# Performance work log

Measured on AMD Instinct MI355X. Metric: run time of the kernel, lower is better.

## Reference

```python
import jax, jax.numpy as jnp
import numpy as np

N_NODES = 50000
N_REL = 256
D_IN = 128
NHID = 128
NHEADS = 2
D_OUT = NHID * NHEADS  # 256
ALPHA = 0.2  # leakyrelu slope


def _l2norm(x, eps=1e-12):
    n = jnp.sqrt(jnp.sum(x * x, axis=1, keepdims=True))
    return x / jnp.maximum(n, eps)


def _gat_layer(x, edge, edge_embed, a, a2, num_nodes, concat):
    """KBGAT-style sparse attention layer.
    x: [N, d_in]; edge: [2, E] (row0=dst, row1=src); edge_embed: [E, d_rel]
    a: [d_out, 2*d_in + d_rel]; a2: [d_out].
    Returns (h, h_raw, rowsum) ~ (x, x_l, x_w) of the original layer.
    """
    d_in = x.shape[1]
    dst, src = edge[0], edge[1]
    # edge_m = a @ cat(x[dst], x[src], edge_embed).T, computed blockwise -> [E, d_out]
    a_d, a_s, a_r = a[:, :d_in], a[:, d_in:2 * d_in], a[:, 2 * d_in:]
    edge_m = x[dst] @ a_d.T + x[src] @ a_s.T + edge_embed @ a_r.T
    # attention logits: exp(-leakyrelu(a2 . edge_m))
    powers = -jax.nn.leaky_relu(edge_m @ a2, negative_slope=ALPHA)  # [E]
    edge_e = jnp.exp(powers)
    rowsum = jax.ops.segment_sum(edge_e, dst, num_segments=num_nodes)  # [N]
    rowsum = jnp.where(rowsum == 0, 1e-12, rowsum)
    h_raw = jax.ops.segment_sum(edge_e[:, None] * edge_m, dst, num_segments=num_nodes)  # [N, d_out]
    h = h_raw / rowsum[:, None]
    if concat:
        h = jax.nn.elu(h)
    return h, h_raw, rowsum[:, None]


def setup_inputs() -> dict:
    key = jax.random.key(0)
    ks = jax.random.split(key, 16)
    E, E_NHOP = 300000, 30000
    xav = lambda k, shp: jax.random.uniform(k, shp, jnp.float32, -1.0, 1.0) * (
        1.414 * np.sqrt(6.0 / (shp[-2] + shp[-1])))
    inp = {
        "entity_embeddings": jax.random.normal(ks[0], (N_NODES, D_IN), jnp.float32),
        "relation_embeddings": jax.random.normal(ks[1], (N_REL, D_IN), jnp.float32),
        # per-head layer-1 attention params (stacked over heads)
        "a1": xav(ks[2], (NHEADS, NHID, 2 * D_IN + D_IN)),
        "a2_1": xav(ks[3], (NHEADS, NHID)),
        "W": xav(ks[4], (D_IN, D_OUT)),          # relation projection in SpGAT
        "a_out": xav(ks[5], (D_OUT, 2 * D_OUT + D_OUT)),
        "a2_out": xav(ks[6], (1, D_OUT))[0],
        "W_entities": xav(ks[7], (D_IN, D_OUT)),
        "batch_inputs": jax.random.randint(ks[8], (4096, 3), 0, N_NODES),
        "edge_list": jax.random.randint(ks[9], (2, E), 0, N_NODES),
        "edge_type": jax.random.randint(ks[10], (E,), 0, N_REL),
        "edge_list_nhop": jax.random.randint(ks[11], (2, E_NHOP), 0, N_NODES),
        "edge_type_nhop": jax.random.randint(ks[12], (E_NHOP, 2), 0, N_REL),
    }
    return inp


def reference(entity_embeddings, relation_embeddings, a1, a2_1, W, a_out, a2_out,
              W_entities, batch_inputs, edge_list, edge_type, edge_list_nhop,
              edge_type_nhop):
    # in-place row normalization of entity embeddings (as in original forward)
    ent = _l2norm(entity_embeddings)
    edge_all = jnp.concatenate([edge_list, edge_list_nhop], axis=1)  # [2, E+Enh]

    # ---- SpGAT layer 1: multi-head over original relation embeddings ----
    edge_embed = relation_embeddings[edge_type]
    edge_embed_nhop = relation_embeddings[edge_type_nhop[:, 0]] + relation_embeddings[edge_type_nhop[:, 1]]
    ee_all = jnp.concatenate([edge_embed, edge_embed_nhop], axis=0)
    heads = [
        _gat_layer(ent, edge_all, ee_all, a1[h], a2_1[h], N_NODES, concat=True)[0]
        for h in range(NHEADS)
    ]
    x = jnp.concatenate(heads, axis=1)  # [N, NHEADS*NHID]

    # ---- relation projection + output attention layer ----
    out_relation_1 = relation_embeddings @ W  # [R, D_OUT]
    ee2 = out_relation_1[edge_type]
    ee2_nhop = out_relation_1[edge_type_nhop[:, 0]] + out_relation_1[edge_type_nhop[:, 1]]
    ee2_all = jnp.concatenate([ee2, ee2_nhop], axis=0)
    xo, x_l, x_w = _gat_layer(x, edge_all, ee2_all, a_out, a2_out, N_NODES, concat=False)
    xo, x_l, x_w = jax.nn.elu(xo), jax.nn.elu(x_l), jax.nn.elu(x_w)

    # ---- residual mask update + normalization ----
    mask = jnp.zeros((N_NODES,), xo.dtype).at[batch_inputs[:, 2]].set(1.0)
    entities_upgraded = ent @ W_entities
    out_entity_1 = entities_upgraded + mask[:, None] * xo
    out_entity_1 = _l2norm(out_entity_1)
    out_entity_l_1 = _l2norm(x_l)
    return (out_entity_1, out_relation_1, out_entity_l_1)
```

## Files before the change

### kernel.cpp

```cpp
#include <hip/hip_runtime.h>
#include <hip/hip_bf16.h>
#include <math.h>

#define N_NODES 50000
#define E1 300000
#define EN 30000
#define ETOT 330000

typedef __hip_bfloat16 bf16;

__device__ __forceinline__ float b2f(bf16 x){ return __bfloat162float(x); }
__device__ __forceinline__ bf16 f2b(float x){ return __float2bfloat16(x); }

__device__ __forceinline__ float ldf(const void* p, long i, bool f32){
  return f32 ? ((const float*)p)[i] : b2f(((const bf16*)p)[i]);
}
__device__ __forceinline__ void stf(void* p, long i, float v, bool f32){
  if (f32) ((float*)p)[i] = v; else ((bf16*)p)[i] = f2b(v);
}
__device__ __forceinline__ void stv4(void* p, long elem, float a, float b,
                                     float c, float d, bool f32){
  if (f32){
    float4 t; t.x=a; t.y=b; t.z=c; t.w=d;
    *reinterpret_cast<float4*>((float*)p + elem) = t;
  } else {
    bf16 t[4] = {f2b(a), f2b(b), f2b(c), f2b(d)};
    *reinterpret_cast<uint2*>((bf16*)p + elem) = *reinterpret_cast<uint2*>(t);
  }
}

template<int NT>
__device__ __forceinline__ float block_sum(float v){
  __shared__ float sm[NT/64];
  #pragma unroll
  for (int o=32;o>0;o>>=1) v += __shfl_down(v,o);
  if ((threadIdx.x & 63)==0) sm[threadIdx.x>>6] = v;
  __syncthreads();
  float t = 0.f;
  #pragma unroll
  for (int w=0;w<NT/64;w++) t += sm[w];
  __syncthreads();
  return t;
}

__global__ void k_detect(const void* __restrict__ emb, int* __restrict__ flag){
  const unsigned short* h = (const unsigned short*)emb;
  int sane = 0;
  for (int i=0;i<128;i++){
    unsigned e = (h[i]>>7)&0xFFu;
    if (e>=112u && e<=143u) sane++;
  }
  *flag = (sane >= 112) ? 0 : 1;
}

__global__ void k_hist(const int* __restrict__ el, const int* __restrict__ eln,
                       int* __restrict__ cnt){
  int i = blockIdx.x*blockDim.x + threadIdx.x;
  if (i < ETOT){
    int dst = (i < E1) ? el[i] : eln[i - E1];
    atomicAdd(cnt + dst, 1);
  }
}

__global__ __launch_bounds__(1024) void k_scan(const int* __restrict__ cnt,
                                               int* __restrict__ rowp,
                                               int* __restrict__ cur){
  __shared__ int part[1024];
  int t = threadIdx.x;
  const int CH = (N_NODES + 1023)/1024;
  int base = t*CH;
  int s = 0;
  for (int i=0;i<CH;i++){ int n = base+i; if (n < N_NODES) s += cnt[n]; }
  part[t] = s;
  __syncthreads();
  for (int o=1;o<1024;o<<=1){
    int u = (t>=o) ? part[t-o] : 0;
    __syncthreads();
    part[t] += u;
    __syncthreads();
  }
  int off = part[t] - s;
  for (int i=0;i<CH;i++){
    int n = base+i;
    if (n < N_NODES){ rowp[n] = off; cur[n] = off; off += cnt[n]; }
  }
  if (t==0) rowp[N_NODES] = ETOT;
}

__global__ void k_fill(const int* __restrict__ el, const int* __restrict__ et,
                       const int* __restrict__ eln, const int* __restrict__ etn,
                       int* __restrict__ cur, int* __restrict__ esrc,
                       int* __restrict__ epak){
  int i = blockIdx.x*blockDim.x + threadIdx.x;
  if (i >= ETOT) return;
  int dst, src, pk;
  if (i < E1){
    dst = el[i]; src = el[E1 + i];
    pk = et[i];
  } else {
    int e = i - E1;
    dst = eln[e]; src = eln[EN + e];
    pk = etn[2*e] | (etn[2*e+1]<<9) | (1<<18);
  }
  int pos = atomicAdd(cur + dst, 1);
  esrc[pos] = src; epak[pos] = pk;
}

__global__ __launch_bounds__(256) void k_gath1(
    const int* __restrict__ rowp, const int* __restrict__ esrc,
    const int* __restrict__ epak,
    const float* __restrict__ pd, const float* __restrict__ ps,
    const float* __restrict__ rp,
    const float* __restrict__ sd, const float* __restrict__ ss,
    const float* __restrict__ sr,
    float* __restrict__ x, int hoff){
  int w = threadIdx.x >> 6, lane = threadIdx.x & 63;
  int n = blockIdx.x*4 + w;
  if (n >= N_NODES) return;
  const float2* ps2 = (const float2*)ps;
  const float2* rp2 = (const float2*)rp;
  float2 acc; acc.x = 0.f; acc.y = 0.f;
  float rs = 0.f;
  float sdn = sd[n];
  int b = rowp[n], e = rowp[n+1];
  for (int i=b;i<e;i++){
    int src = esrc[i], pk = epak[i];
    int t0 = pk & 511, t1 = (pk>>9)&511, has2 = (pk>>18)&1;
    float srv = sr[t0] + (has2 ? sr[t1] : 0.f);
    float score = sdn + ss[src] + srv;
    float lr = score > 0.f ? score : 0.2f*score;
    float wgt = expf(-lr);
    rs += wgt;
    float2 v  = ps2[(long)src*64 + lane];
    float2 r1 = rp2[(long)t0*64 + lane];
    v.x += r1.x; v.y += r1.y;
    if (has2){ float2 r2v = rp2[(long)t1*64 + lane]; v.x += r2v.x; v.y += r2v.y; }
    acc.x += wgt*v.x; acc.y += wgt*v.y;
  }
  float denom = (rs == 0.f) ? 1e-12f : rs;
  float2 pdv = ((const float2*)pd)[(long)n*64 + lane];
  float hr0 = rs*pdv.x + acc.x, hr1 = rs*pdv.y + acc.y;
  float h0 = hr0/denom; h0 = h0 > 0.f ? h0 : (expf(h0) - 1.f);
  float h1 = hr1/denom; h1 = h1 > 0.f ? h1 : (expf(h1) - 1.f);
  float2 o; o.x = h0; o.y = h1;
  *reinterpret_cast<float2*>(x + (long)n*256 + hoff + lane*2) = o;
}

__global__ __launch_bounds__(256) void k_gath2(
    const int* __restrict__ rowp, const int* __restrict__ esrc,
    const int* __restrict__ epak,
    const float* __restrict__ p2d, const float* __restrict__ ps,
    const float* __restrict__ rp,
    const float* __restrict__ sd, const float* __restrict__ ss,
    const float* __restrict__ sr,
    const float* __restrict__ eu, const float* __restrict__ mask,
    const int* __restrict__ flag, void* __restrict__ out){
  bool f32 = flag[0] != 0;
  int w = threadIdx.x >> 6, lane = threadIdx.x & 63;
  int n = blockIdx.x*4 + w;
  if (n >= N_NODES) return;
  const float4* ps4 = (const float4*)ps;
  const float4* rp4 = (const float4*)rp;
  float4 acc; acc.x=acc.y=acc.z=acc.w=0.f;
  float rs = 0.f;
  float sdn = sd[n];
  int b = rowp[n], e = rowp[n+1];
  for (int i=b;i<e;i++){
    int src = esrc[i], pk = epak[i];
    int t0 = pk & 511, t1 = (pk>>9)&511, has2 = (pk>>18)&1;
    float srv = sr[t0] + (has2 ? sr[t1] : 0.f);
    float score = sdn + ss[src] + srv;
    float lr = score > 0.f ? score : 0.2f*score;
    float wgt = expf(-lr);
    rs += wgt;
    float4 v  = ps4[(long)src*64 + lane];
    float4 r1 = rp4[(long)t0*64 + lane];
    v.x += r1.x; v.y += r1.y; v.z += r1.z; v.w += r1.w;
    if (has2){
      float4 r2v = rp4[(long)t1*64 + lane];
      v.x += r2v.x; v.y += r2v.y; v.z += r2v.z; v.w += r2v.w;
    }
    acc.x += wgt*v.x; acc.y += wgt*v.y; acc.z += wgt*v.z; acc.w += wgt*v.w;
  }
  float denom = (rs == 0.f) ? 1e-12f : rs;
  float mk = mask[n];
  float4 pdv = ((const float4*)p2d)[(long)n*64 + lane];
  float4 euv = ((const float4*)eu)[(long)n*64 + lane];
  float av[4] = {acc.x, acc.y, acc.z, acc.w};
  float pv[4] = {pdv.x, pdv.y, pdv.z, pdv.w};
  float ev[4] = {euv.x, euv.y, euv.z, euv.w};
  float val[4], xl[4];
  float n1 = 0.f, n2 = 0.f;
  #pragma unroll
  for (int m=0;m<4;m++){
    float hr = rs*pv[m] + av[m];
    float xo = hr/denom; xo = xo > 0.f ? xo : (expf(xo) - 1.f);
    float l  = hr > 0.f ? hr : (expf(hr) - 1.f);
    float v  = ev[m] + mk*xo;
    val[m] = v; xl[m] = l;
    n1 += v*v; n2 += l*l;
  }
  #pragma unroll
  for (int o=32;o>0;o>>=1){ n1 += __shfl_xor(n1,o); n2 += __shfl_xor(n2,o); }
  float i1 = 1.f/fmaxf(sqrtf(n1), 1e-12f);
  float i2 = 1.f/fmaxf(sqrtf(n2), 1e-12f);
  stv4(out, (long)n*256 + lane*4,
       val[0]*i1, val[1]*i1, val[2]*i1, val[3]*i1, f32);
  stv4(out, 12865536L + (long)n*256 + lane*4,
       xl[0]*i2, xl[1]*i2, xl[2]*i2, xl[3]*i2, f32);
}

__global__ void k_rel2(const void* __restrict__ rel, const void* __restrict__ W,
                       const int* __restrict__ flag,
                       float* __restrict__ r2, void* __restrict__ out){
  bool f32 = flag[0] != 0;
  int t = blockIdx.x, j = threadIdx.x;
  __shared__ float rs_[128];
  if (j < 128) rs_[j] = ldf(rel, (long)t*128 + j, f32);
  __syncthreads();
  float acc = 0.f;
  #pragma unroll 4
  for (int k=0;k<128;k++) acc += rs_[k]*ldf(W, (long)k*256 + j, f32);
  r2[(long)t*256+j] = acc;
  stf(out, 12800000L + (long)t*256 + j, acc, f32);
}

__global__ void k_trF(const void* __restrict__ src, const int* __restrict__ flag,
                      long bias, long jstride, int J, float* __restrict__ dst){
  bool f32 = flag[0] != 0;
  int k = blockIdx.x, j = threadIdx.x;
  dst[(long)k*J + j] = ldf(src, bias + (long)j*jstride + k, f32);
}

__global__ void k_cvtF(const void* __restrict__ src, const int* __restrict__ flag,
                       int n, float* __restrict__ dst){
  bool f32 = flag[0] != 0;
  int i = blockIdx.x*blockDim.x + threadIdx.x;
  if (i < n) dst[i] = ldf(src, i, f32);
}

template<int NT, int K, int BM, int NORM, int DUAL, int SCORE, int XDUAL>
__global__ __launch_bounds__(NT) void k_gnp(
    const void* __restrict__ X, const int* __restrict__ flag, int N,
    const float* __restrict__ WT1, const float* __restrict__ WT2,
    const void* __restrict__ a2, long a2bias,
    float* __restrict__ O1, float* __restrict__ O2,
    float* __restrict__ s1, float* __restrict__ s2, int ldc){
  __shared__ __align__(16) float xs[BM][K];
  __shared__ float rsc[BM];
  const int NW = NT/64;
  __shared__ float red1[BM][NW];
  __shared__ float red2[BM][NW];
  int t = threadIdx.x;
  int n0 = blockIdx.x * BM;
  bool xf32 = XDUAL ? (flag[0] != 0) : true;

  for (int idx = t; idx < BM*K; idx += NT){
    int m = idx / K, k = idx - m*K;
    int n = n0 + m;
    xs[m][k] = (n < N) ? ldf(X, (long)n*K + k, xf32) : 0.f;
  }
  __syncthreads();

  if (NORM){
    const int NPR = NT / BM;
    int r = t / NPR, l = t - r*NPR;
    float ssq = 0.f;
    #pragma unroll
    for (int k = l; k < K; k += NPR){ float v = xs[r][k]; ssq += v*v; }
    #pragma unroll
    for (int o = NPR>>1; o > 0; o >>= 1) ssq += __shfl_xor(ssq, o);
    if (l == 0) rsc[r] = 1.f / fmaxf(sqrtf(ssq), 1e-12f);
    __syncthreads();
    for (int idx = t; idx < BM*K; idx += NT){
      int m = idx / K, k = idx - m*K;
      xs[m][k] *= rsc[m];
    }
    __syncthreads();
  }

  float a1c[BM], a2c[BM];
  #pragma unroll
  for (int m=0;m<BM;m++){ a1c[m]=0.f; a2c[m]=0.f; }
  const float4* xs4 = reinterpret_cast<const float4*>(&xs[0][0]);
  #pragma unroll 2
  for (int k0=0;k0<K;k0+=4){
    float w1a = WT1[(long)(k0+0)*NT + t];
    float w1b = WT1[(long)(k0+1)*NT + t];
    float w1c = WT1[(long)(k0+2)*NT + t];
    float w1d = WT1[(long)(k0+3)*NT + t];
    float w2a=0.f,w2b=0.f,w2c=0.f,w2d=0.f;
    if (DUAL){
      w2a = WT2[(long)(k0+0)*NT + t];
      w2b = WT2[(long)(k0+1)*NT + t];
      w2c = WT2[(long)(k0+2)*NT + t];
      w2d = WT2[(long)(k0+3)*NT + t];
    }
    #pragma unroll
    for (int m=0;m<BM;m++){
      float4 xv = xs4[(m*K + k0) >> 2];
      a1c[m] += xv.x*w1a + xv.y*w1b + xv.z*w1c + xv.w*w1d;
      if (DUAL) a2c[m] += xv.x*w2a + xv.y*w2b + xv.z*w2c + xv.w*w2d;
    }
  }

  #pragma unroll
  for (int m=0;m<BM;m++){
    int n = n0 + m;
    if (n < N){
      O1[(long)n*ldc + t] = a1c[m];
      if (DUAL) O2[(long)n*ldc + t] = a2c[m];
    }
  }

  if (SCORE){
    bool af32 = flag[0] != 0;
    float a2v = ldf(a2, a2bias + t, af32);
    int w = t >> 6, lane = t & 63;
    #pragma unroll
    for (int m=0;m<BM;m++){
      float v1 = a1c[m]*a2v;
      float v2 = DUAL ? a2c[m]*a2v : 0.f;
      #pragma unroll
      for (int o=32;o>0;o>>=1){ v1 += __shfl_down(v1,o); v2 += __shfl_down(v2,o); }
      if (lane==0){ red1[m][w]=v1; red2[m][w]=v2; }
    }
    __syncthreads();
    if (t < BM && n0 + t < N){
      float v1=0.f, v2=0.f;
      #pragma unroll
      for (int ww=0;ww<NW;ww++){ v1+=red1[t][ww]; v2+=red2[t][ww]; }
      s1[n0+t] = v1;
      if (DUAL) s2[n0+t] = v2;
    }
  }
}

__global__ void k_mask(const int* __restrict__ bi, float* __restrict__ mask){
  int i = blockIdx.x*blockDim.x + threadIdx.x;
  if (i < 4096) mask[bi[i*3 + 2]] = 1.f;
}

extern "C" void kernel_launch(void* const* d_in, const int* in_sizes, int n_in,
                              void* d_out, int out_size, void* d_ws, size_t ws_size,
                              hipStream_t stream) {
  const void* emb = d_in[0];
  const void* rel = d_in[1];
  const void* a1b = d_in[2];
  const void* a21 = d_in[3];
  const void* W   = d_in[4];
  const void* aout= d_in[5];
  const void* a2o = d_in[6];
  const void* We  = d_in[7];
  const int* bi   = (const int*)d_in[8];
  const int* el   = (const int*)d_in[9];
  const int* et   = (const int*)d_in[10];
  const int* eln  = (const int*)d_in[11];
  const int* etn  = (const int*)d_in[12];
  float* ws = (float*)d_ws;

  const size_t PD_=0, PS_=6400000;
  const size_t P2D_=0;
  const size_t CNT_=12800000, ROWP_=12860000, ESRC_=12920000, EPAK_=13260000;
  const size_t TW_=19200000;
  const size_t X_=25600000;
  const size_t P2S_=38400000;
  const size_t SD_=51250000, SS_=51300000, S2D_=51350000,
               S2S_=51400000, MK_=51500000,
               RP1_=51550000, SR1_=51590000, R2_=51600000, RP2_=51670000,
               SR2_=51740000, FLAG_=51750000;
  int* flag = (int*)(ws + FLAG_);
  int* cnt  = (int*)(ws + CNT_);
  int* rowp = (int*)(ws + ROWP_);
  int* esrc = (int*)(ws + ESRC_);
  int* epak = (int*)(ws + EPAK_);

  k_detect<<<1,1,0,stream>>>(emb, flag);

  hipMemsetAsync(ws+MK_,  0, (size_t)50000*sizeof(float), stream);
  hipMemsetAsync(cnt,     0, (size_t)50000*sizeof(int), stream);

  k_hist<<<(ETOT+255)/256,256,0,stream>>>(el, eln, cnt);
  k_scan<<<1,1024,0,stream>>>(cnt, rowp, cnt);
  k_fill<<<(ETOT+255)/256,256,0,stream>>>(el, et, eln, etn, cnt, esrc, epak);

  k_trF<<<128,128,0,stream>>>(a1b, flag, 0L,          384L, 128, ws+TW_);
  k_trF<<<128,128,0,stream>>>(a1b, flag, 128L,        384L, 128, ws+TW_+16384);
  k_trF<<<128,128,0,stream>>>(a1b, flag, 49152L,      384L, 128, ws+TW_+32768);
  k_trF<<<128,128,0,stream>>>(a1b, flag, 49152L+128L, 384L, 128, ws+TW_+49152);
  k_trF<<<128,128,0,stream>>>(a1b, flag, 256L,        384L, 128, ws+TW_+65536);
  k_trF<<<128,128,0,stream>>>(a1b, flag, 49152L+256L, 384L, 128, ws+TW_+81920);

  k_gnp<128,128,16,1,1,1,1><<<(N_NODES+15)/16,128,0,stream>>>(
      emb, flag, N_NODES, ws+TW_, ws+TW_+16384, a21, 0L,
      ws+PD_, ws+PS_, ws+SD_, ws+SS_, 128);
  k_gnp<128,128,16,0,0,1,1><<<16,128,0,stream>>>(
      rel, flag, 256, ws+TW_+65536, nullptr, a21, 0L,
      ws+RP1_, nullptr, ws+SR1_, nullptr, 128);
  k_gath1<<<(N_NODES+3)/4,256,0,stream>>>(rowp, esrc, epak,
      ws+PD_, ws+PS_, ws+RP1_, ws+SD_, ws+SS_, ws+SR1_, ws+X_, 0);

  k_gnp<128,128,16,1,1,1,1><<<(N_NODES+15)/16,128,0,stream>>>(
      emb, flag, N_NODES, ws+TW_+32768, ws+TW_+49152, a21, 128L,
      ws+PD_, ws+PS_, ws+SD_, ws+SS_, 128);
  k_gnp<128,128,16,0,0,1,1><<<16,128,0,stream>>>(
      rel, flag, 256, ws+TW_+81920, nullptr, a21, 128L,
      ws+RP1_, nullptr, ws+SR1_, nullptr, 128);
  k_gath1<<<(N_NODES+3)/4,256,0,stream>>>(rowp, esrc, epak,
      ws+PD_, ws+PS_, ws+RP1_, ws+SD_, ws+SS_, ws+SR1_, ws+X_, 128);

  k_rel2<<<256,256,0,stream>>>(rel, W, flag, ws+R2_, d_out);

  k_trF<<<256,256,0,stream>>>(aout, flag, 0L,   768L, 256, ws+TW_);
  k_trF<<<256,256,0,stream>>>(aout, flag, 256L, 768L, 256, ws+TW_+65536);
  k_trF<<<256,256,0,stream>>>(aout, flag, 512L, 768L, 256, ws+TW_+131072);

  k_gnp<256,256,16,0,0,1,0><<<16,256,0,stream>>>(
      ws+R2_, flag, 256, ws+TW_+131072, nullptr, a2o, 0L,
      ws+RP2_, nullptr, ws+SR2_, nullptr, 256);

  k_gnp<256,256,16,0,1,1,0><<<(N_NODES+15)/16,256,0,stream>>>(
      ws+X_, flag, N_NODES, ws+TW_, ws+TW_+65536, a2o, 0L,
      ws+P2D_, ws+P2S_, ws+S2D_, ws+S2S_, 256);

  k_cvtF<<<128,256,0,stream>>>(We, flag, 32768, ws+RP1_);
  k_mask<<<16,256,0,stream>>>(bi, ws+MK_);
  k_gnp<256,128,16,1,0,0,1><<<(N_NODES+15)/16,256,0,stream>>>(
      emb, flag, N_NODES, ws+RP1_, nullptr, nullptr, 0L,
      ws+X_, nullptr, nullptr, nullptr, 256);

  k_gath2<<<(N_NODES+3)/4,256,0,stream>>>(rowp, esrc, epak,
      ws+P2D_, ws+P2S_, ws+RP2_, ws+S2D_, ws+S2S_, ws+SR2_,
      ws+X_, ws+MK_, flag, d_out);
}
```

Baseline: 1.106 ms.

## Register-tile node projection GEMM: split rows across waves, multiple columns per lane

Restructures the dense projection kernel so each wave owns a subset of the block's rows and each lane computes 2 or 4 adjacent output columns. Weights are loaded as float2/float4 vectors, outputs are stored vectorized, and the attention score reduction becomes a single in-wave shuffle with no shared-memory pass or barrier. The intent is to cut redundant shared-memory reads and weight loads per FMA. Layer-1 launches move from 128 to 256 threads. The weight layout is unchanged (row-major by column), so lane-contiguous column groups map directly onto it.

```diff
diff --git a/kernel.cpp b/kernel.cpp
--- a/kernel.cpp
+++ b/kernel.cpp
@@ -239,19 +239,21 @@
   if (i < n) dst[i] = ldf(src, i, f32);
 }
 
-template<int NT, int K, int BM, int NORM, int DUAL, int SCORE, int XDUAL>
+template<int NT, int K, int BM, int NCOL, int NORM, int DUAL, int SCORE, int XDUAL>
 __global__ __launch_bounds__(NT) void k_gnp(
     const void* __restrict__ X, const int* __restrict__ flag, int N,
     const float* __restrict__ WT1, const float* __restrict__ WT2,
     const void* __restrict__ a2, long a2bias,
     float* __restrict__ O1, float* __restrict__ O2,
-    float* __restrict__ s1, float* __restrict__ s2, int ldc){
+    float* __restrict__ s1, float* __restrict__ s2){
+  const int COLS  = 64*NCOL;
+  const int WAVES = NT/64;
+  const int RW    = BM/WAVES;
   __shared__ __align__(16) float xs[BM][K];
   __shared__ float rsc[BM];
-  const int NW = NT/64;
-  __shared__ float red1[BM][NW];
-  __shared__ float red2[BM][NW];
   int t = threadIdx.x;
+  int wv = t >> 6, ln = t & 63;
+  int r0 = wv * RW;
   int n0 = blockIdx.x * BM;
   bool xf32 = XDUAL ? (flag[0] != 0) : true;
 
@@ -279,59 +281,95 @@
     __syncthreads();
   }
 
-  float a1c[BM], a2c[BM];
-  #pragma unroll
-  for (int m=0;m<BM;m++){ a1c[m]=0.f; a2c[m]=0.f; }
-  const float4* xs4 = reinterpret_cast<const float4*>(&xs[0][0]);
-  #pragma unroll 2
+  float a1c[RW][NCOL], a2c[RW][NCOL];
+  #pragma unroll
+  for (int m=0;m<RW;m++)
+    #pragma unroll
+    for (int c=0;c<NCOL;c++){ a1c[m][c]=0.f; a2c[m][c]=0.f; }
+
   for (int k0=0;k0<K;k0+=4){
-    float w1a = WT1[(long)(k0+0)*NT + t];
-    float w1b = WT1[(long)(k0+1)*NT + t];
-    float w1c = WT1[(long)(k0+2)*NT + t];
-    float w1d = WT1[(long)(k0+3)*NT + t];
-    float w2a=0.f,w2b=0.f,w2c=0.f,w2d=0.f;
-    if (DUAL){
-      w2a = WT2[(long)(k0+0)*NT + t];
-      w2b = WT2[(long)(k0+1)*NT + t];
-      w2c = WT2[(long)(k0+2)*NT + t];
-      w2d = WT2[(long)(k0+3)*NT + t];
-    }
-    #pragma unroll
-    for (int m=0;m<BM;m++){
-      float4 xv = xs4[(m*K + k0) >> 2];
-      a1c[m] += xv.x*w1a + xv.y*w1b + xv.z*w1c + xv.w*w1d;
-      if (DUAL) a2c[m] += xv.x*w2a + xv.y*w2b + xv.z*w2c + xv.w*w2d;
-    }
-  }
-
-  #pragma unroll
-  for (int m=0;m<BM;m++){
-    int n = n0 + m;
+    float w1v[4][NCOL], w2v[4][NCOL];
+    #pragma unroll
+    for (int i=0;i<4;i++){
+      const float* p1 = WT1 + (long)(k0+i)*COLS + ln*NCOL;
+      if constexpr (NCOL==4){
+        float4 v = *reinterpret_cast<const float4*>(p1);
+        w1v[i][0]=v.x; w1v[i][1]=v.y; w1v[i][2]=v.z; w1v[i][3]=v.w;
+      } else {
+        float2 v = *reinterpret_cast<const float2*>(p1);
+        w1v[i][0]=v.x; w1v[i][1]=v.y;
+      }
+      if (DUAL){
+        const float* p2 = WT2 + (long)(k0+i)*COLS + ln*NCOL;
+        if constexpr (NCOL==4){
+          float4 v = *reinterpret_cast<const float4*>(p2);
+          w2v[i][0]=v.x; w2v[i][1]=v.y; w2v[i][2]=v.z; w2v[i][3]=v.w;
+        } else {
+          float2 v = *reinterpret_cast<const float2*>(p2);
+          w2v[i][0]=v.x; w2v[i][1]=v.y;
+        }
+      }
+    }
+    #pragma unroll
+    for (int m=0;m<RW;m++){
+      float4 xv = *reinterpret_cast<const float4*>(&xs[r0+m][k0]);
+      #pragma unroll
+      for (int c=0;c<NCOL;c++){
+        a1c[m][c] += xv.x*w1v[0][c] + xv.y*w1v[1][c] + xv.z*w1v[2][c] + xv.w*w1v[3][c];
+        if (DUAL)
+          a2c[m][c] += xv.x*w2v[0][c] + xv.y*w2v[1][c] + xv.z*w2v[2][c] + xv.w*w2v[3][c];
+      }
+    }
+  }
+
+  #pragma unroll
+  for (int m=0;m<RW;m++){
+    int n = n0 + r0 + m;
     if (n < N){
-      O1[(long)n*ldc + t] = a1c[m];
-      if (DUAL) O2[(long)n*ldc + t] = a2c[m];
+      float* o1 = O1 + (long)n*COLS + ln*NCOL;
+      if constexpr (NCOL==4){
+        float4 v; v.x=a1c[m][0]; v.y=a1c[m][1]; v.z=a1c[m][2]; v.w=a1c[m][3];
+        *reinterpret_cast<float4*>(o1) = v;
+      } else {
+        float2 v; v.x=a1c[m][0]; v.y=a1c[m][1];
+        *reinterpret_cast<float2*>(o1) = v;
+      }
+      if (DUAL){
+        float* o2 = O2 + (long)n*COLS + ln*NCOL;
+        if constexpr (NCOL==4){
+          float4 v; v.x=a2c[m][0]; v.y=a2c[m][1]; v.z=a2c[m][2]; v.w=a2c[m][3];
+          *reinterpret_cast<float4*>(o2) = v;
+        } else {
+          float2 v; v.x=a2c[m][0]; v.y=a2c[m][1];
+          *reinterpret_cast<float2*>(o2) = v;
+        }
+      }
     }
   }
 
   if (SCORE){
     bool af32 = flag[0] != 0;
-    float a2v = ldf(a2, a2bias + t, af32);
-    int w = t >> 6, lane = t & 63;
-    #pragma unroll
-    for (int m=0;m<BM;m++){
-      float v1 = a1c[m]*a2v;
-      float v2 = DUAL ? a2c[m]*a2v : 0.f;
+    float a2v[NCOL];
+    #pragma unroll
+    for (int c=0;c<NCOL;c++) a2v[c] = ldf(a2, a2bias + ln*NCOL + c, af32);
+    #pragma unroll
+    for (int m=0;m<RW;m++){
+      float v1 = 0.f, v2 = 0.f;
       #pragma unroll
-      for (int o=32;o>0;o>>=1){ v1 += __shfl_down(v1,o); v2 += __shfl_down(v2,o); }
-      if (lane==0){ red1[m][w]=v1; red2[m][w]=v2; }
-    }
-    __syncthreads();
-    if (t < BM && n0 + t < N){
-      float v1=0.f, v2=0.f;
+      for (int c=0;c<NCOL;c++){
+        v1 += a1c[m][c]*a2v[c];
+        if (DUAL) v2 += a2c[m][c]*a2v[c];
+      }
       #pragma unroll
-      for (int ww=0;ww<NW;ww++){ v1+=red1[t][ww]; v2+=red2[t][ww]; }
-      s1[n0+t] = v1;
-      if (DUAL) s2[n0+t] = v2;
+      for (int o=32;o>0;o>>=1){
+        v1 += __shfl_down(v1,o);
+        if (DUAL) v2 += __shfl_down(v2,o);
+      }
+      int n = n0 + r0 + m;
+      if (ln==0 && n < N){
+        s1[n] = v1;
+        if (DUAL) s2[n] = v2;
+      }
     }
   }
 }
@@ -391,21 +429,21 @@
   k_trF<<<128,128,0,stream>>>(a1b, flag, 256L,        384L, 128, ws+TW_+65536);
   k_trF<<<128,128,0,stream>>>(a1b, flag, 49152L+256L, 384L, 128, ws+TW_+81920);
 
-  k_gnp<128,128,16,1,1,1,1><<<(N_NODES+15)/16,128,0,stream>>>(
+  k_gnp<256,128,16,2,1,1,1,1><<<(N_NODES+15)/16,256,0,stream>>>(
       emb, flag, N_NODES, ws+TW_, ws+TW_+16384, a21, 0L,
-      ws+PD_, ws+PS_, ws+SD_, ws+SS_, 128);
-  k_gnp<128,128,16,0,0,1,1><<<16,128,0,stream>>>(
+      ws+PD_, ws+PS_, ws+SD_, ws+SS_);
+  k_gnp<256,128,16,2,0,0,1,1><<<16,256,0,stream>>>(
       rel, flag, 256, ws+TW_+65536, nullptr, a21, 0L,
-      ws+RP1_, nullptr, ws+SR1_, nullptr, 128);
+      ws+RP1_, nullptr, ws+SR1_, nullptr);
   k_gath1<<<(N_NODES+3)/4,256,0,stream>>>(rowp, esrc, epak,
       ws+PD_, ws+PS_, ws+RP1_, ws+SD_, ws+SS_, ws+SR1_, ws+X_, 0);
 
-  k_gnp<128,128,16,1,1,1,1><<<(N_NODES+15)/16,128,0,stream>>>(
+  k_gnp<256,128,16,2,1,1,1,1><<<(N_NODES+15)/16,256,0,stream>>>(
       emb, flag, N_NODES, ws+TW_+32768, ws+TW_+49152, a21, 128L,
-      ws+PD_, ws+PS_, ws+SD_, ws+SS_, 128);
-  k_gnp<128,128,16,0,0,1,1><<<16,128,0,stream>>>(
+      ws+PD_, ws+PS_, ws+SD_, ws+SS_);
+  k_gnp<256,128,16,2,0,0,1,1><<<16,256,0,stream>>>(
       rel, flag, 256, ws+TW_+81920, nullptr, a21, 128L,
-      ws+RP1_, nullptr, ws+SR1_, nullptr, 128);
+      ws+RP1_, nullptr, ws+SR1_, nullptr);
   k_gath1<<<(N_NODES+3)/4,256,0,stream>>>(rowp, esrc, epak,
       ws+PD_, ws+PS_, ws+RP1_, ws+SD_, ws+SS_, ws+SR1_, ws+X_, 128);
 
@@ -415,19 +453,19 @@
   k_trF<<<256,256,0,stream>>>(aout, flag, 256L, 768L, 256, ws+TW_+65536);
   k_trF<<<256,256,0,stream>>>(aout, flag, 512L, 768L, 256, ws+TW_+131072);
 
-  k_gnp<256,256,16,0,0,1,0><<<16,256,0,stream>>>(
+  k_gnp<256,256,16,4,0,0,1,0><<<16,256,0,stream>>>(
       ws+R2_, flag, 256, ws+TW_+131072, nullptr, a2o, 0L,
-      ws+RP2_, nullptr, ws+SR2_, nullptr, 256);
-
-  k_gnp<256,256,16,0,1,1,0><<<(N_NODES+15)/16,256,0,stream>>>(
+      ws+RP2_, nullptr, ws+SR2_, nullptr);
+
+  k_gnp<256,256,16,4,0,1,1,0><<<(N_NODES+15)/16,256,0,stream>>>(
       ws+X_, flag, N_NODES, ws+TW_, ws+TW_+65536, a2o, 0L,
-      ws+P2D_, ws+P2S_, ws+S2D_, ws+S2S_, 256);
+      ws+P2D_, ws+P2S_, ws+S2D_, ws+S2S_);
 
   k_cvtF<<<128,256,0,stream>>>(We, flag, 32768, ws+RP1_);
   k_mask<<<16,256,0,stream>>>(bi, ws+MK_);
-  k_gnp<256,128,16,1,0,0,1><<<(N_NODES+15)/16,256,0,stream>>>(
+  k_gnp<256,128,16,4,1,0,0,1><<<(N_NODES+15)/16,256,0,stream>>>(
       emb, flag, N_NODES, ws+RP1_, nullptr, nullptr, 0L,
-      ws+X_, nullptr, nullptr, nullptr, 256);
+      ws+X_, nullptr, nullptr, nullptr);
 
   k_gath2<<<(N_NODES+3)/4,256,0,stream>>>(rowp, esrc, epak,
       ws+P2D_, ws+P2S_, ws+RP2_, ws+S2D_, ws+S2S_, ws+SR2_,
```

After: 1.155 ms. +4.5%, slower.
